# Optimization experiments

Hardware: AMD Instinct MI355X
Metric: run time of the kernel (lower is better)

The kernel has to match this reference:

```python
import jax, jax.numpy as jnp
import numpy as np

LOSS_WEIGHT = 1.0

def setup_inputs() -> dict:
    key = jax.random.key(0)
    k1, k2 = jax.random.split(key)
    B, M, N = 4, 8192, 8192
    pred_colors = jax.random.uniform(k1, (B, M, 3), dtype=jnp.float32)
    gt_colors = jax.random.uniform(k2, (B, N, 3), dtype=jnp.float32)
    return {"pred_colors": pred_colors, "gt_colors": gt_colors}

def reference(pred_colors, gt_colors):
    # torch.cdist(p=2): Euclidean distance matrix [B, M, N]
    # ||a-b||^2 = ||a||^2 + ||b||^2 - 2 a.b
    a2 = jnp.sum(pred_colors * pred_colors, axis=-1)  # [B, M]
    b2 = jnp.sum(gt_colors * gt_colors, axis=-1)      # [B, N]
    ab = jnp.einsum('bmd,bnd->bmn', pred_colors, gt_colors)  # [B, M, N]
    d2 = a2[:, :, None] + b2[:, None, :] - 2.0 * ab
    dists = jnp.sqrt(jnp.maximum(d2, 0.0))
    min_dists = jnp.min(dists, axis=2)  # [B, M]
    return min_dists.mean() * LOSS_WEIGHT
```

## Files before the change

kernel.cpp:

```cpp
#include <hip/hip_runtime.h>
#include <math.h>


constexpr int B  = 4;
constexpr int M  = 8192;
constexpr int N  = 8192;
constexpr int BM = B * M;
constexpr int G  = 16;
constexpr int NC = G * G * G;
constexpr float H = 1.0f / G;

__device__ __forceinline__ int cell_of(float x) {
  int c = (int)(x * (float)G);
  return c < 0 ? 0 : (c > G - 1 ? G - 1 : c);
}

__global__ __launch_bounds__(1024)
void k_bin(const float* __restrict__ gt, float4* __restrict__ sorted,
           int* __restrict__ cell_start, int* __restrict__ fail_count,
           float* __restrict__ out)
{
  const int b = blockIdx.x, t = threadIdx.x;
  const int lane = t & 63, wv = t >> 6;
  if (b == 0 && t == 0) { out[0] = 0.0f; fail_count[0] = 0; }
  __shared__ int cnt[NC];
  __shared__ int wtot[16];

  for (int c = t; c < NC; c += 1024) cnt[c] = 0;
  __syncthreads();

  float px[8], py[8], pz[8]; int pc[8];
  const float* g = gt + (size_t)b * N * 3;
#pragma unroll
  for (int i = 0; i < 8; ++i) {
    const int idx = t + i * 1024;
    px[i] = g[idx * 3 + 0];
    py[i] = g[idx * 3 + 1];
    pz[i] = g[idx * 3 + 2];
    pc[i] = (cell_of(pz[i]) * G + cell_of(py[i])) * G + cell_of(px[i]);
    atomicAdd(&cnt[pc[i]], 1);
  }
  __syncthreads();

  const int i0 = 4 * t;
  int v0 = cnt[i0], v1 = cnt[i0 + 1], v2 = cnt[i0 + 2], v3 = cnt[i0 + 3];
  const int own = v0 + v1 + v2 + v3;
  int s = own;
  for (int off = 1; off < 64; off <<= 1) {
    int nb = __shfl_up(s, off, 64);
    if (lane >= off) s += nb;
  }
  if (lane == 63) wtot[wv] = s;
  __syncthreads();
  if (t == 0) {
    int run = 0;
#pragma unroll
    for (int w = 0; w < 16; ++w) { int x = wtot[w]; wtot[w] = run; run += x; }
  }
  __syncthreads();
  const int excl = s - own + wtot[wv];
  cnt[i0]     = excl;
  cnt[i0 + 1] = excl + v0;
  cnt[i0 + 2] = excl + v0 + v1;
  cnt[i0 + 3] = excl + v0 + v1 + v2;
  __syncthreads();

  int* cs = cell_start + b * (NC + 1);
  for (int c = t; c < NC; c += 1024) cs[c] = cnt[c];
  if (t == 0) cs[NC] = N;
  __syncthreads();

  float4* dst = sorted + (size_t)b * N;
#pragma unroll
  for (int i = 0; i < 8; ++i) {
    const int pos = atomicAdd(&cnt[pc[i]], 1);
    dst[pos] = make_float4(px[i], py[i], pz[i], 0.0f);
  }
}

__global__ __launch_bounds__(256)
void k_query(const float* __restrict__ pred, const float4* __restrict__ sorted,
             const int* __restrict__ cell_start, int* __restrict__ fail_count,
             int* __restrict__ fail_list, float* __restrict__ out)
{
  const int tid = blockIdx.x * 256 + threadIdx.x;
  const int p = tid >> 2;
  const int l = tid & 3;
  const int b = p >> 13;
  const float* a = pred + (size_t)p * 3;
  const float ax = a[0], ay = a[1], az = a[2];
  const int qi = cell_of(ax), qj = cell_of(ay), qk = cell_of(az);
  const float4* pts = sorted + (size_t)b * N;
  const int* cs = cell_start + b * (NC + 1);
  const int x0  = qi - 1 < 0 ? 0 : qi - 1;
  const int x1e = (qi + 1 > G - 1 ? G - 1 : qi + 1) + 1;

  int rs[3], re[3];
#pragma unroll
  for (int j = 0; j < 3; ++j) {
    const int rr = l + 4 * j;
    if (rr < 9) {
      const int dz = rr / 3 - 1, dy = rr % 3 - 1;
      const int z = qk + dz < 0 ? 0 : (qk + dz > G - 1 ? G - 1 : qk + dz);
      const int y = qj + dy < 0 ? 0 : (qj + dy > G - 1 ? G - 1 : qj + dy);
      const int cb = (z * G + y) * G;
      rs[j] = cs[cb + x0];
      re[j] = cs[cb + x1e];
    } else { rs[j] = 0; re[j] = 0; }
  }

  float best2 = 3.0e38f;
#pragma unroll
  for (int j = 0; j < 3; ++j) {
    int i = rs[j];
    const int e = re[j];
    for (; i + 4 <= e; i += 4) {
      const float4 q0 = pts[i], q1 = pts[i + 1], q2 = pts[i + 2], q3 = pts[i + 3];
      const float d0 = fmaf(ax - q0.x, ax - q0.x, fmaf(ay - q0.y, ay - q0.y, (az - q0.z) * (az - q0.z)));
      const float d1 = fmaf(ax - q1.x, ax - q1.x, fmaf(ay - q1.y, ay - q1.y, (az - q1.z) * (az - q1.z)));
      const float d2 = fmaf(ax - q2.x, ax - q2.x, fmaf(ay - q2.y, ay - q2.y, (az - q2.z) * (az - q2.z)));
      const float d3 = fmaf(ax - q3.x, ax - q3.x, fmaf(ay - q3.y, ay - q3.y, (az - q3.z) * (az - q3.z)));
      best2 = fminf(best2, fminf(fminf(d0, d1), fminf(d2, d3)));
    }
    for (; i < e; ++i) {
      const float4 q = pts[i];
      const float dx = ax - q.x, dy = ay - q.y, dz = az - q.z;
      best2 = fminf(best2, fmaf(dx, dx, fmaf(dy, dy, dz * dz)));
    }
  }

  best2 = fminf(best2, __shfl_xor(best2, 1, 64));
  best2 = fminf(best2, __shfl_xor(best2, 2, 64));

  float val = 0.0f;
  if (l == 0) {
    if (best2 <= H * H) {
      val = sqrtf(best2) * (1.0f / BM);
    } else {
      fail_list[atomicAdd(fail_count, 1)] = p;
    }
  }

  for (int off = 32; off; off >>= 1) val += __shfl_down(val, off, 64);
  __shared__ float wsum[4];
  if ((threadIdx.x & 63) == 0) wsum[threadIdx.x >> 6] = val;
  __syncthreads();
  if (threadIdx.x == 0) atomicAdd(out, wsum[0] + wsum[1] + wsum[2] + wsum[3]);
}

__global__ __launch_bounds__(256)
void k_fix(const float* __restrict__ pred, const float4* __restrict__ sorted,
           const int* __restrict__ fail_count, const int* __restrict__ fail_list,
           float* __restrict__ out)
{
  const int cnt = fail_count[0];
  __shared__ float wmin[4];
  for (int f = blockIdx.x; f < cnt; f += gridDim.x) {
    const int p = fail_list[f];
    const int b = p >> 13;
    const float* a = pred + (size_t)p * 3;
    const float ax = a[0], ay = a[1], az = a[2];
    const float4* pts = sorted + (size_t)b * N;
    float best2 = 3.0e38f;
#pragma unroll 4
    for (int i = threadIdx.x; i < N; i += 256) {
      const float4 q = pts[i];
      const float dx = ax - q.x, dy = ay - q.y, dz = az - q.z;
      best2 = fminf(best2, fmaf(dx, dx, fmaf(dy, dy, dz * dz)));
    }
#pragma unroll
    for (int off = 32; off; off >>= 1)
      best2 = fminf(best2, __shfl_xor(best2, off, 64));
    if ((threadIdx.x & 63) == 0) wmin[threadIdx.x >> 6] = best2;
    __syncthreads();
    if (threadIdx.x == 0) {
      const float m = fminf(fminf(wmin[0], wmin[1]), fminf(wmin[2], wmin[3]));
      atomicAdd(out, sqrtf(m) * (1.0f / BM));
    }
    __syncthreads();
  }
}

__global__ __launch_bounds__(256)
void k_brute(const float* __restrict__ pred, const float* __restrict__ gt,
             float* __restrict__ out)
{
  constexpr int TPB = 256, RPT = 8, PPB = TPB * RPT, MBLK = M / PPB;
  const int mb = blockIdx.x % MBLK, b = blockIdx.x / MBLK, t = threadIdx.x;
  __shared__ float4 tile[1024];
  float cx[RPT], cy[RPT], cz[RPT], mn[RPT];
  const int mbase = mb * PPB + t;
#pragma unroll
  for (int r = 0; r < RPT; ++r) {
    const float* a = pred + ((size_t)b * M + (mbase + r * TPB)) * 3;
    cx[r] = -2.0f * a[0]; cy[r] = -2.0f * a[1]; cz[r] = -2.0f * a[2];
    mn[r] = 3.0e38f;
  }
  for (int n0 = 0; n0 < N; n0 += 1024) {
    __syncthreads();
    for (int i = t; i < 1024; i += TPB) {
      const float* gp = gt + ((size_t)b * N + (n0 + i)) * 3;
      float gx = gp[0], gy = gp[1], gz = gp[2];
      tile[i] = make_float4(gx, gy, gz, fmaf(gx, gx, fmaf(gy, gy, gz * gz)));
    }
    __syncthreads();
#pragma unroll 2
    for (int n = 0; n < 1024; n += 2) {
      const float4 g0 = tile[n], g1 = tile[n + 1];
#pragma unroll
      for (int r = 0; r < RPT; ++r) {
        float s0 = fmaf(cx[r], g0.x, fmaf(cy[r], g0.y, fmaf(cz[r], g0.z, g0.w)));
        float s1 = fmaf(cx[r], g1.x, fmaf(cy[r], g1.y, fmaf(cz[r], g1.z, g1.w)));
        mn[r] = fminf(fminf(s0, s1), mn[r]);
      }
    }
  }
  float sum = 0.0f;
#pragma unroll
  for (int r = 0; r < RPT; ++r) {
    const float* a = pred + ((size_t)b * M + (mbase + r * TPB)) * 3;
    float a2 = fmaf(a[0], a[0], fmaf(a[1], a[1], a[2] * a[2]));
    sum += sqrtf(fmaxf(a2 + mn[r], 0.0f)) * (1.0f / BM);
  }
  for (int off = 32; off; off >>= 1) sum += __shfl_down(sum, off, 64);
  __shared__ float wsum[4];
  if ((t & 63) == 0) wsum[t >> 6] = sum;
  __syncthreads();
  if (t == 0) atomicAdd(out, wsum[0] + wsum[1] + wsum[2] + wsum[3]);
}

extern "C" void kernel_launch(void* const* d_in, const int* in_sizes, int n_in,
                              void* d_out, int out_size, void* d_ws, size_t ws_size,
                              hipStream_t stream)
{
  const float* pred = (const float*)d_in[0];
  const float* gt   = (const float*)d_in[1];
  float* out = (float*)d_out;

  const size_t sz_sorted = (size_t)B * N * sizeof(float4);
  const size_t sz_cs     = (size_t)B * (NC + 1) * sizeof(int);
  const size_t sz_fc     = 16;
  const size_t sz_fl     = (size_t)BM * sizeof(int);
  if (ws_size >= sz_sorted + sz_cs + sz_fc + sz_fl) {
    char* w = (char*)d_ws;
    float4* sorted  = (float4*)w;                 w += sz_sorted;
    int* cell_start = (int*)w;                    w += sz_cs;
    int* fail_count = (int*)w;                    w += sz_fc;
    int* fail_list  = (int*)w;
    k_bin<<<dim3(B), dim3(1024), 0, stream>>>(gt, sorted, cell_start, fail_count, out);
    k_query<<<dim3(BM * 4 / 256), dim3(256), 0, stream>>>(pred, sorted, cell_start,
                                                          fail_count, fail_list, out);
    k_fix<<<dim3(256), dim3(256), 0, stream>>>(pred, sorted, fail_count, fail_list, out);
  } else {
    hipMemsetAsync(out, 0, sizeof(float), stream);
    k_brute<<<dim3(B * (M / 2048)), dim3(256), 0, stream>>>(pred, gt, out);
  }
}
```

Baseline: 82.54 us.

## Split grid binning into parallel count, scan, and scatter kernels

Replaces the single 4-block binning kernel, which used one 1024-thread block per batch and LDS atomics, with three kernels: a wide global-atomic count, a per-batch scan, and a wide scatter using global cursor atomics. The aim is to spread the binning work across many CUs instead of four. In exchange it adds a memset and two extra kernel launches, plus global atomic contention on the cell counters. It also needs more workspace, so the brute-force fallback may be taken if the workspace is too small.

```diff
diff --git a/kernel.cpp b/kernel.cpp
--- a/kernel.cpp
+++ b/kernel.cpp
@@ -15,35 +15,29 @@
   return c < 0 ? 0 : (c > G - 1 ? G - 1 : c);
 }
 
+__global__ __launch_bounds__(256)
+void k_count(const float* __restrict__ gt, int* __restrict__ cnt,
+             int* __restrict__ fail_count, float* __restrict__ out)
+{
+  const int p = blockIdx.x * 256 + threadIdx.x;
+  if (p == 0) { out[0] = 0.0f; fail_count[0] = 0; }
+  const int b = p >> 13, idx = p & (N - 1);
+  const float* g = gt + ((size_t)b * N + idx) * 3;
+  const int c = (cell_of(g[2]) * G + cell_of(g[1])) * G + cell_of(g[0]);
+  atomicAdd(&cnt[b * NC + c], 1);
+}
+
 __global__ __launch_bounds__(1024)
-void k_bin(const float* __restrict__ gt, float4* __restrict__ sorted,
-           int* __restrict__ cell_start, int* __restrict__ fail_count,
-           float* __restrict__ out)
+void k_scan(const int* __restrict__ cnt, int* __restrict__ cell_start,
+            int* __restrict__ cursor)
 {
   const int b = blockIdx.x, t = threadIdx.x;
   const int lane = t & 63, wv = t >> 6;
-  if (b == 0 && t == 0) { out[0] = 0.0f; fail_count[0] = 0; }
-  __shared__ int cnt[NC];
   __shared__ int wtot[16];
 
-  for (int c = t; c < NC; c += 1024) cnt[c] = 0;
-  __syncthreads();
-
-  float px[8], py[8], pz[8]; int pc[8];
-  const float* g = gt + (size_t)b * N * 3;
-#pragma unroll
-  for (int i = 0; i < 8; ++i) {
-    const int idx = t + i * 1024;
-    px[i] = g[idx * 3 + 0];
-    py[i] = g[idx * 3 + 1];
-    pz[i] = g[idx * 3 + 2];
-    pc[i] = (cell_of(pz[i]) * G + cell_of(py[i])) * G + cell_of(px[i]);
-    atomicAdd(&cnt[pc[i]], 1);
-  }
-  __syncthreads();
-
   const int i0 = 4 * t;
-  int v0 = cnt[i0], v1 = cnt[i0 + 1], v2 = cnt[i0 + 2], v3 = cnt[i0 + 3];
+  const int* src = cnt + b * NC;
+  int v0 = src[i0], v1 = src[i0 + 1], v2 = src[i0 + 2], v3 = src[i0 + 3];
   const int own = v0 + v1 + v2 + v3;
   int s = own;
   for (int off = 1; off < 64; off <<= 1) {
@@ -59,23 +53,26 @@
   }
   __syncthreads();
   const int excl = s - own + wtot[wv];
-  cnt[i0]     = excl;
-  cnt[i0 + 1] = excl + v0;
-  cnt[i0 + 2] = excl + v0 + v1;
-  cnt[i0 + 3] = excl + v0 + v1 + v2;
-  __syncthreads();
 
   int* cs = cell_start + b * (NC + 1);
-  for (int c = t; c < NC; c += 1024) cs[c] = cnt[c];
+  int* cu = cursor + b * NC;
+  const int e0 = excl, e1 = excl + v0, e2 = excl + v0 + v1, e3 = excl + v0 + v1 + v2;
+  cs[i0] = e0; cs[i0 + 1] = e1; cs[i0 + 2] = e2; cs[i0 + 3] = e3;
+  cu[i0] = e0; cu[i0 + 1] = e1; cu[i0 + 2] = e2; cu[i0 + 3] = e3;
   if (t == 0) cs[NC] = N;
-  __syncthreads();
-
-  float4* dst = sorted + (size_t)b * N;
-#pragma unroll
-  for (int i = 0; i < 8; ++i) {
-    const int pos = atomicAdd(&cnt[pc[i]], 1);
-    dst[pos] = make_float4(px[i], py[i], pz[i], 0.0f);
-  }
+}
+
+__global__ __launch_bounds__(256)
+void k_scatter(const float* __restrict__ gt, int* __restrict__ cursor,
+               float4* __restrict__ sorted)
+{
+  const int p = blockIdx.x * 256 + threadIdx.x;
+  const int b = p >> 13, idx = p & (N - 1);
+  const float* g = gt + ((size_t)b * N + idx) * 3;
+  const float x = g[0], y = g[1], z = g[2];
+  const int c = (cell_of(z) * G + cell_of(y)) * G + cell_of(x);
+  const int pos = atomicAdd(&cursor[b * NC + c], 1);
+  sorted[(size_t)b * N + pos] = make_float4(x, y, z, 0.0f);
 }
 
 __global__ __launch_bounds__(256)
@@ -239,18 +236,28 @@
 
   const size_t sz_sorted = (size_t)B * N * sizeof(float4);
   const size_t sz_cs     = (size_t)B * (NC + 1) * sizeof(int);
+  const size_t sz_cnt    = (size_t)B * NC * sizeof(int);
+  const size_t sz_cur    = (size_t)B * NC * sizeof(int);
   const size_t sz_fc     = 16;
   const size_t sz_fl     = (size_t)BM * sizeof(int);
-  if (ws_size >= sz_sorted + sz_cs + sz_fc + sz_fl) {
+  const size_t need = sz_sorted + sz_cs + sz_cnt + sz_cur + sz_fc + sz_fl;
+
+  if (ws_size >= need) {
     char* w = (char*)d_ws;
-    float4* sorted  = (float4*)w;                 w += sz_sorted;
-    int* cell_start = (int*)w;                    w += sz_cs;
-    int* fail_count = (int*)w;                    w += sz_fc;
+    float4* sorted  = (float4*)w;  w += sz_sorted;
+    int* cell_start = (int*)w;     w += sz_cs;
+    int* cnt        = (int*)w;     w += sz_cnt;
+    int* cursor     = (int*)w;     w += sz_cur;
+    int* fail_count = (int*)w;     w += sz_fc;
     int* fail_list  = (int*)w;
-    k_bin<<<dim3(B), dim3(1024), 0, stream>>>(gt, sorted, cell_start, fail_count, out);
-    k_query<<<dim3(BM * 4 / 256), dim3(256), 0, stream>>>(pred, sorted, cell_start,
-                                                          fail_count, fail_list, out);
-    k_fix<<<dim3(256), dim3(256), 0, stream>>>(pred, sorted, fail_count, fail_list, out);
+
+    hipMemsetAsync(cnt, 0, sz_cnt, stream);
+    k_count  <<<dim3(BM / 256), dim3(256),  0, stream>>>(gt, cnt, fail_count, out);
+    k_scan   <<<dim3(B),        dim3(1024), 0, stream>>>(cnt, cell_start, cursor);
+    k_scatter<<<dim3(BM / 256), dim3(256),  0, stream>>>(gt, cursor, sorted);
+    k_query  <<<dim3(BM * 4 / 256), dim3(256), 0, stream>>>(pred, sorted, cell_start,
+                                                            fail_count, fail_list, out);
+    k_fix    <<<dim3(256), dim3(256), 0, stream>>>(pred, sorted, fail_count, fail_list, out);
   } else {
     hipMemsetAsync(out, 0, sizeof(float), stream);
     k_brute<<<dim3(B * (M / 2048)), dim3(256), 0, stream>>>(pred, gt, out);
```

New measurement: 84.57 us. +2.5%, slower.
